# Kernel optimization log

Hardware: AMD Instinct MI355X
Metric: run time of the kernel (lower is better)

Reference implementation:

```python
import jax, jax.numpy as jnp
import numpy as np

CODEBOOK_SIZE = 1024
EMBEDDING_DIM = 64


def setup_inputs() -> dict:
    key = jax.random.key(0)
    k_in, k_cb = jax.random.split(key)
    # latent feature (batch, embedding_dim, length)
    input = jax.random.normal(k_in, (16, EMBEDDING_DIM, 8192), dtype=jnp.float32)
    # learned codebook table (codebook_size, embedding_dim)
    codebook = jax.random.normal(k_cb, (CODEBOOK_SIZE, EMBEDDING_DIM), dtype=jnp.float32)
    return {"input": input, "codebook": codebook}


def reference(input, codebook):
    # input: (B, D, T); codebook: (K, D)
    B, D = input.shape[0], input.shape[1]
    spatial = input.shape[2:]
    # move embedding dim last and flatten tokens: (B*T, D)
    x = jnp.moveaxis(input, 1, -1).reshape(-1, D)
    x_sq = jnp.sum(x * x, axis=-1, keepdims=True)            # (N, 1)
    e_sq = jnp.sum(codebook * codebook, axis=-1)             # (K,)
    dist = x_sq - 2.0 * (x @ codebook.T) + e_sq[None, :]     # (N, K)
    indices = jnp.argmin(dist, axis=-1)                      # (N,)
    quantized = jnp.take(codebook, indices, axis=0)          # (N, D)
    # reshape back: output (B, D, *spatial), indices (B, *spatial)
    out = jnp.moveaxis(quantized.reshape((B,) + spatial + (D,)), -1, 1)
    idx = indices.reshape((B,) + spatial)
    return out, idx
```

## Files before the change

### kernel.cpp

```cpp
#include <hip/hip_runtime.h>
#include <float.h>

#define K_CODES 1024
#define DIM 64
#define T_LEN 8192
#define N_TOK 131072
#define LO_SCALE 2048.0f
#define LO_INV   (1.0f / 2048.0f)

typedef _Float16 half8 __attribute__((ext_vector_type(8)));
typedef float    f32x4 __attribute__((ext_vector_type(4)));

#define MFMA16(a, b, c) __builtin_amdgcn_mfma_f32_16x16x32_f16((a), (b), (c), 0, 0, 0)

__global__ void vq_prep(const float* __restrict__ cb,
                        _Float16* __restrict__ w,
                        float* __restrict__ wesq) {
    __shared__ float part[128];
    const int ct   = blockIdx.x;
    const int r    = threadIdx.x;
    const int halF = r >> 7;
    const int rr   = r & 127;
    const int q    = rr >> 4;
    const int code = rr & 15;

    const float* src = cb + (size_t)(ct * 16 + code) * DIM + q * 8;
    float4 v0 = *reinterpret_cast<const float4*>(src);
    float4 v1 = *reinterpret_cast<const float4*>(src + 4);
    float x[8] = {v0.x, v0.y, v0.z, v0.w, v1.x, v1.y, v1.z, v1.w};

    half8 o;
    float psum = 0.0f;
    #pragma unroll
    for (int j = 0; j < 8; ++j) {
        _Float16 h = (_Float16)x[j];
        o[j] = halF ? (_Float16)((x[j] - (float)h) * LO_SCALE) : h;
        psum = fmaf(x[j], x[j], psum);
    }
    *reinterpret_cast<half8*>(w + (size_t)ct * 2048 + halF * 1024 + q * 128 + code * 8) = o;

    if (halF == 0) part[rr] = psum;
    __syncthreads();
    if (r < 16) {
        float s = 0.0f;
        #pragma unroll
        for (int q2 = 0; q2 < 8; ++q2) s += part[q2 * 16 + r];
        wesq[ct * 16 + r] = s;
    }
}

__global__ __launch_bounds__(256, 4)
void vq_main(const float* __restrict__ in,
             const float* __restrict__ cb,
             const _Float16* __restrict__ w,
             const float* __restrict__ wesq,
             float* __restrict__ out) {
    __shared__ int idx_s[128];

    const int tid  = threadIdx.x;
    const int wave = tid >> 6;
    const int lane = tid & 63;
    const int lo4  = lane & 15;
    const int quad = lane >> 4;

    const int strip = blockIdx.x * 128 + wave * 32;
    const int b  = strip >> 13;
    const int t0 = strip & 8191;

    const float* xin = in + (size_t)b * DIM * T_LEN + t0;
    half8 a_hi[2][2], a_lo[2][2];
    #pragma unroll
    for (int mt = 0; mt < 2; ++mt) {
        #pragma unroll
        for (int s = 0; s < 2; ++s) {
            half8 hh, ll;
            #pragma unroll
            for (int j = 0; j < 8; ++j) {
                const int d = s * 32 + quad * 8 + j;
                float xv = -2.0f * xin[(size_t)d * T_LEN + mt * 16 + lo4];
                _Float16 h = (_Float16)xv;
                hh[j] = h;
                ll[j] = (_Float16)((xv - (float)h) * LO_SCALE);
            }
            a_hi[mt][s] = hh;
            a_lo[mt][s] = ll;
        }
    }

    float best[8];
    int   bidx[8];
    #pragma unroll
    for (int i = 0; i < 8; ++i) { best[i] = FLT_MAX; bidx[i] = 0; }

    const _Float16* wb = w + (size_t)lane * 8;

    half8 Ah0, Ah1, Al0, Al1, Bh0, Bh1, Bl0, Bl1;
    float Ae, Be;

    auto loadB = [&](int ct, half8& h0, half8& h1, half8& l0, half8& l1, float& es) {
        const _Float16* p = wb + (size_t)ct * 2048;
        h0 = *reinterpret_cast<const half8*>(p);
        h1 = *reinterpret_cast<const half8*>(p + 512);
        l0 = *reinterpret_cast<const half8*>(p + 1024);
        l1 = *reinterpret_cast<const half8*>(p + 1536);
        es = wesq[ct * 16 + lo4];
    };
    auto step = [&](const half8& h0, const half8& h1, const half8& l0,
                    const half8& l1, float es, int ct) {
        const int code = ct * 16 + lo4;
        #pragma unroll
        for (int mt = 0; mt < 2; ++mt) {
            f32x4 c1 = {es, es, es, es};
            f32x4 c2 = {0.f, 0.f, 0.f, 0.f};
            c1 = MFMA16(a_hi[mt][0], h0, c1);
            c1 = MFMA16(a_hi[mt][1], h1, c1);
            c2 = MFMA16(a_lo[mt][0], h0, c2);
            c2 = MFMA16(a_lo[mt][1], h1, c2);
            c2 = MFMA16(a_hi[mt][0], l0, c2);
            c2 = MFMA16(a_hi[mt][1], l1, c2);
            #pragma unroll
            for (int r = 0; r < 4; ++r) {
                float sc = fmaf(c2[r], LO_INV, c1[r]);
                const int i = mt * 4 + r;
                bool lt = sc < best[i];
                best[i] = lt ? sc : best[i];
                bidx[i] = lt ? code : bidx[i];
            }
        }
    };

    loadB(0, Ah0, Ah1, Al0, Al1, Ae);
    loadB(1, Bh0, Bh1, Bl0, Bl1, Be);
    for (int p = 0; p < 31; ++p) {
        step(Ah0, Ah1, Al0, Al1, Ae, 2 * p);
        loadB(2 * p + 2, Ah0, Ah1, Al0, Al1, Ae);
        step(Bh0, Bh1, Bl0, Bl1, Be, 2 * p + 1);
        loadB(2 * p + 3, Bh0, Bh1, Bl0, Bl1, Be);
    }
    step(Ah0, Ah1, Al0, Al1, Ae, 62);
    step(Bh0, Bh1, Bl0, Bl1, Be, 63);

    #pragma unroll
    for (int i = 0; i < 8; ++i) {
        float s = best[i];
        int  ix = bidx[i];
        #pragma unroll
        for (int off = 1; off < 16; off <<= 1) {
            float s2 = __shfl_xor(s, off, 64);
            int  ix2 = __shfl_xor(ix, off, 64);
            bool take = (s2 < s) || (s2 == s && ix2 < ix);
            s  = take ? s2 : s;
            ix = take ? ix2 : ix;
        }
        if (lo4 == 0) {
            idx_s[wave * 32 + (i >> 2) * 16 + quad * 4 + (i & 3)] = ix;
        }
    }
    __syncthreads();

    const int tok_local = tid & 127;
    const int dhalf = tid >> 7;
    const int token = blockIdx.x * 128 + tok_local;
    const int tb = token >> 13;
    const int tt = token & 8191;
    const int my_idx = idx_s[tok_local];

    if (dhalf == 0)
        out[(size_t)N_TOK * DIM + token] = (float)my_idx;

    const float* crow = cb + (size_t)my_idx * DIM + dhalf * 32;
    float* outv = out + (size_t)tb * DIM * T_LEN + (size_t)(dhalf * 32) * T_LEN + tt;
    #pragma unroll
    for (int d0 = 0; d0 < 32; d0 += 4) {
        float4 v = *reinterpret_cast<const float4*>(crow + d0);
        outv[(size_t)(d0 + 0) * T_LEN] = v.x;
        outv[(size_t)(d0 + 1) * T_LEN] = v.y;
        outv[(size_t)(d0 + 2) * T_LEN] = v.z;
        outv[(size_t)(d0 + 3) * T_LEN] = v.w;
    }
}

extern "C" void kernel_launch(void* const* d_in, const int* in_sizes, int n_in,
                              void* d_out, int out_size, void* d_ws, size_t ws_size,
                              hipStream_t stream) {
    const float* in = (const float*)d_in[0];
    const float* cb = (const float*)d_in[1];
    float* out = (float*)d_out;

    _Float16* w   = (_Float16*)d_ws;
    float*   wesq = (float*)((char*)d_ws + 64 * 4096);

    vq_prep<<<dim3(64), dim3(256), 0, stream>>>(cb, w, wesq);
    vq_main<<<dim3(N_TOK / 128), dim3(256), 0, stream>>>(in, cb, w, wesq, out);
}
```

Before: 134.0 us.

## Stage codebook tiles in LDS via async global-to-LDS double buffering

Instead of every wave loading the same split-fp16 codebook tiles from global memory into registers, the block cooperatively copies 4 tiles at a time into a double-buffered LDS area using global_load_lds. Each wave then reads its fragments from LDS, with one barrier per period. The codebook squared norms are also preloaded into LDS. This cuts redundant L2/global traffic by sharing loads across the 4 waves. The cost is extra LDS use (about 36 KB per block, which may limit occupancy), LDS read latency and per-period barriers.

Result: slower. 139.5 us (+4.1%).

```diff
diff --git a/kernel.cpp b/kernel.cpp
--- a/kernel.cpp
+++ b/kernel.cpp
@@ -12,6 +12,17 @@
 typedef float    f32x4 __attribute__((ext_vector_type(4)));
 
 #define MFMA16(a, b, c) __builtin_amdgcn_mfma_f32_16x16x32_f16((a), (b), (c), 0, 0, 0)
+
+typedef __attribute__((address_space(3))) void* as3_void;
+typedef const __attribute__((address_space(1))) void* as1_cvoid;
+
+__device__ inline void async_16B(const void* g, void* l) {
+#if __has_builtin(__builtin_amdgcn_global_load_lds)
+    __builtin_amdgcn_global_load_lds((as1_cvoid)g, (as3_void)l, 16, 0, 0);
+#else
+    *(float4*)l = *(const float4*)g;
+#endif
+}
 
 __global__ void vq_prep(const float* __restrict__ cb,
                         _Float16* __restrict__ w,
@@ -55,13 +66,17 @@
              const _Float16* __restrict__ w,
              const float* __restrict__ wesq,
              float* __restrict__ out) {
-    __shared__ int idx_s[128];
+    __shared__ __align__(16) _Float16 bt[2][4][2048];
+    __shared__ float esq_s[K_CODES];
+    __shared__ int   idx_s[128];
 
     const int tid  = threadIdx.x;
     const int wave = tid >> 6;
     const int lane = tid & 63;
     const int lo4  = lane & 15;
     const int quad = lane >> 4;
+
+    for (int k = tid; k < K_CODES; k += 256) esq_s[k] = wesq[k];
 
     const int strip = blockIdx.x * 128 + wave * 32;
     const int b  = strip >> 13;
@@ -92,53 +107,55 @@
     #pragma unroll
     for (int i = 0; i < 8; ++i) { best[i] = FLT_MAX; bidx[i] = 0; }
 
-    const _Float16* wb = w + (size_t)lane * 8;
-
-    half8 Ah0, Ah1, Al0, Al1, Bh0, Bh1, Bl0, Bl1;
-    float Ae, Be;
-
-    auto loadB = [&](int ct, half8& h0, half8& h1, half8& l0, half8& l1, float& es) {
-        const _Float16* p = wb + (size_t)ct * 2048;
-        h0 = *reinterpret_cast<const half8*>(p);
-        h1 = *reinterpret_cast<const half8*>(p + 512);
-        l0 = *reinterpret_cast<const half8*>(p + 1024);
-        l1 = *reinterpret_cast<const half8*>(p + 1536);
-        es = wesq[ct * 16 + lo4];
+    const char* wbytes = (const char*)w;
+    auto stage = [&](int per, int buf) {
+        const char* src = wbytes + (size_t)per * 16384 + lane * 16;
+        char* dst = (char*)&bt[buf][0][0] + lane * 16;
+        #pragma unroll
+        for (int i = 0; i < 4; ++i) {
+            const int c = (wave + i * 4) * 1024;
+            async_16B(src + c, dst + c);
+        }
     };
-    auto step = [&](const half8& h0, const half8& h1, const half8& l0,
-                    const half8& l1, float es, int ct) {
-        const int code = ct * 16 + lo4;
-        #pragma unroll
-        for (int mt = 0; mt < 2; ++mt) {
-            f32x4 c1 = {es, es, es, es};
-            f32x4 c2 = {0.f, 0.f, 0.f, 0.f};
-            c1 = MFMA16(a_hi[mt][0], h0, c1);
-            c1 = MFMA16(a_hi[mt][1], h1, c1);
-            c2 = MFMA16(a_lo[mt][0], h0, c2);
-            c2 = MFMA16(a_lo[mt][1], h1, c2);
-            c2 = MFMA16(a_hi[mt][0], l0, c2);
-            c2 = MFMA16(a_hi[mt][1], l1, c2);
+
+    stage(0, 0);
+    __syncthreads();
+
+    for (int per = 0; per < 16; ++per) {
+        const int buf = per & 1;
+        if (per < 15) stage(per + 1, buf ^ 1);
+        #pragma unroll
+        for (int j = 0; j < 4; ++j) {
+            const int ct = per * 4 + j;
+            const _Float16* tp = &bt[buf][j][lane * 8];
+            half8 h0 = *reinterpret_cast<const half8*>(tp);
+            half8 h1 = *reinterpret_cast<const half8*>(tp + 512);
+            half8 l0 = *reinterpret_cast<const half8*>(tp + 1024);
+            half8 l1 = *reinterpret_cast<const half8*>(tp + 1536);
+            const float es = esq_s[ct * 16 + lo4];
+            const int code = ct * 16 + lo4;
             #pragma unroll
-            for (int r = 0; r < 4; ++r) {
-                float sc = fmaf(c2[r], LO_INV, c1[r]);
-                const int i = mt * 4 + r;
-                bool lt = sc < best[i];
-                best[i] = lt ? sc : best[i];
-                bidx[i] = lt ? code : bidx[i];
+            for (int mt = 0; mt < 2; ++mt) {
+                f32x4 c1 = {es, es, es, es};
+                f32x4 c2 = {0.f, 0.f, 0.f, 0.f};
+                c1 = MFMA16(a_hi[mt][0], h0, c1);
+                c1 = MFMA16(a_hi[mt][1], h1, c1);
+                c2 = MFMA16(a_lo[mt][0], h0, c2);
+                c2 = MFMA16(a_lo[mt][1], h1, c2);
+                c2 = MFMA16(a_hi[mt][0], l0, c2);
+                c2 = MFMA16(a_hi[mt][1], l1, c2);
+                #pragma unroll
+                for (int r = 0; r < 4; ++r) {
+                    float sc = fmaf(c2[r], LO_INV, c1[r]);
+                    const int i = mt * 4 + r;
+                    bool lt = sc < best[i];
+                    best[i] = lt ? sc : best[i];
+                    bidx[i] = lt ? code : bidx[i];
+                }
             }
         }
-    };
-
-    loadB(0, Ah0, Ah1, Al0, Al1, Ae);
-    loadB(1, Bh0, Bh1, Bl0, Bl1, Be);
-    for (int p = 0; p < 31; ++p) {
-        step(Ah0, Ah1, Al0, Al1, Ae, 2 * p);
-        loadB(2 * p + 2, Ah0, Ah1, Al0, Al1, Ae);
-        step(Bh0, Bh1, Bl0, Bl1, Be, 2 * p + 1);
-        loadB(2 * p + 3, Bh0, Bh1, Bl0, Bl1, Be);
-    }
-    step(Ah0, Ah1, Al0, Al1, Ae, 62);
-    step(Bh0, Bh1, Bl0, Bl1, Be, 63);
+        __syncthreads();
+    }
 
     #pragma unroll
     for (int i = 0; i < 8; ++i) {
```

## Double tokens per wave, fold hi/lo split into one scaled accumulator, stage esq in LDS

Applied to the files above, without the earlier changes.

Each wave now handles 64 tokens (4 M-tiles) instead of 32, so every codebook B-fragment loaded from global memory is reused across twice as many MFMAs. The two accumulator chains (hi and lo, combined with an fmaf) become a single chain: the high part of the input is pre-scaled by 2048 and the codebook norms are stored pre-scaled, so the argmin works on scaled distances without the per-element combine. Codebook norms are staged in shared memory, and the grid is halved with launch bounds relaxed to allow more registers. The costs are higher register pressure and lower occupancy. Scaling the high fp16 part by 2048 could also overflow fp16 for large inputs.

New measurement: 128.2 us. 1.05x faster.

```diff
diff --git a/kernel.cpp b/kernel.cpp
--- a/kernel.cpp
+++ b/kernel.cpp
@@ -6,7 +6,6 @@
 #define T_LEN 8192
 #define N_TOK 131072
 #define LO_SCALE 2048.0f
-#define LO_INV   (1.0f / 2048.0f)
 
 typedef _Float16 half8 __attribute__((ext_vector_type(8)));
 typedef float    f32x4 __attribute__((ext_vector_type(4)));
@@ -45,17 +44,18 @@
         float s = 0.0f;
         #pragma unroll
         for (int q2 = 0; q2 < 8; ++q2) s += part[q2 * 16 + r];
-        wesq[ct * 16 + r] = s;
+        wesq[ct * 16 + r] = s * LO_SCALE;
     }
 }
 
-__global__ __launch_bounds__(256, 4)
+__global__ __launch_bounds__(256, 2)
 void vq_main(const float* __restrict__ in,
              const float* __restrict__ cb,
              const _Float16* __restrict__ w,
              const float* __restrict__ wesq,
              float* __restrict__ out) {
-    __shared__ int idx_s[128];
+    __shared__ float esq_s[K_CODES];
+    __shared__ int   idx_s[256];
 
     const int tid  = threadIdx.x;
     const int wave = tid >> 6;
@@ -63,64 +63,67 @@
     const int lo4  = lane & 15;
     const int quad = lane >> 4;
 
-    const int strip = blockIdx.x * 128 + wave * 32;
+    for (int k = tid; k < K_CODES; k += 256) esq_s[k] = wesq[k];
+    __syncthreads();
+
+    const int strip = blockIdx.x * 256 + wave * 64;
     const int b  = strip >> 13;
     const int t0 = strip & 8191;
 
     const float* xin = in + (size_t)b * DIM * T_LEN + t0;
-    half8 a_hi[2][2], a_lo[2][2];
+    half8 a_h[4][2], a_hs[4][2], a_l[4][2];
     #pragma unroll
-    for (int mt = 0; mt < 2; ++mt) {
+    for (int mt = 0; mt < 4; ++mt) {
         #pragma unroll
         for (int s = 0; s < 2; ++s) {
-            half8 hh, ll;
+            half8 hh, hs, ll;
             #pragma unroll
             for (int j = 0; j < 8; ++j) {
                 const int d = s * 32 + quad * 8 + j;
                 float xv = -2.0f * xin[(size_t)d * T_LEN + mt * 16 + lo4];
                 _Float16 h = (_Float16)xv;
                 hh[j] = h;
+                hs[j] = (_Float16)((float)h * LO_SCALE);
                 ll[j] = (_Float16)((xv - (float)h) * LO_SCALE);
             }
-            a_hi[mt][s] = hh;
-            a_lo[mt][s] = ll;
+            a_h[mt][s] = hh;
+            a_hs[mt][s] = hs;
+            a_l[mt][s] = ll;
         }
     }
 
-    float best[8];
-    int   bidx[8];
+    float best[16];
+    int   bidx[16];
     #pragma unroll
-    for (int i = 0; i < 8; ++i) { best[i] = FLT_MAX; bidx[i] = 0; }
+    for (int i = 0; i < 16; ++i) { best[i] = FLT_MAX; bidx[i] = 0; }
 
     const _Float16* wb = w + (size_t)lane * 8;
 
     half8 Ah0, Ah1, Al0, Al1, Bh0, Bh1, Bl0, Bl1;
     float Ae, Be;
-
     auto loadB = [&](int ct, half8& h0, half8& h1, half8& l0, half8& l1, float& es) {
         const _Float16* p = wb + (size_t)ct * 2048;
         h0 = *reinterpret_cast<const half8*>(p);
         h1 = *reinterpret_cast<const half8*>(p + 512);
         l0 = *reinterpret_cast<const half8*>(p + 1024);
         l1 = *reinterpret_cast<const half8*>(p + 1536);
-        es = wesq[ct * 16 + lo4];
+        es = esq_s[ct * 16 + lo4];
     };
     auto step = [&](const half8& h0, const half8& h1, const half8& l0,
                     const half8& l1, float es, int ct) {
         const int code = ct * 16 + lo4;
         #pragma unroll
-        for (int mt = 0; mt < 2; ++mt) {
-            f32x4 c1 = {es, es, es, es};
-            f32x4 c2 = {0.f, 0.f, 0.f, 0.f};
-            c1 = MFMA16(a_hi[mt][0], h0, c1);
-            c1 = MFMA16(a_hi[mt][1], h1, c1);
-            c2 = MFMA16(a_lo[mt][0], h0, c2);
-            c2 = MFMA16(a_lo[mt][1], h1, c2);
-            c2 = MFMA16(a_hi[mt][0], l0, c2);
-            c2 = MFMA16(a_hi[mt][1], l1, c2);
+        for (int mt = 0; mt < 4; ++mt) {
+            f32x4 c = {es, es, es, es};
+            c = MFMA16(a_hs[mt][0], h0, c);
+            c = MFMA16(a_hs[mt][1], h1, c);
+            c = MFMA16(a_h[mt][0], l0, c);
+            c = MFMA16(a_h[mt][1], l1, c);
+            c = MFMA16(a_l[mt][0], h0, c);
+            c = MFMA16(a_l[mt][1], h1, c);
             #pragma unroll
             for (int r = 0; r < 4; ++r) {
-                float sc = fmaf(c2[r], LO_INV, c1[r]);
+                float sc = c[r];
                 const int i = mt * 4 + r;
                 bool lt = sc < best[i];
                 best[i] = lt ? sc : best[i];
@@ -141,7 +144,7 @@
     step(Bh0, Bh1, Bl0, Bl1, Be, 63);
 
     #pragma unroll
-    for (int i = 0; i < 8; ++i) {
+    for (int i = 0; i < 16; ++i) {
         float s = best[i];
         int  ix = bidx[i];
         #pragma unroll
@@ -153,25 +156,22 @@
             ix = take ? ix2 : ix;
         }
         if (lo4 == 0) {
-            idx_s[wave * 32 + (i >> 2) * 16 + quad * 4 + (i & 3)] = ix;
+            idx_s[wave * 64 + (i >> 2) * 16 + quad * 4 + (i & 3)] = ix;
         }
     }
     __syncthreads();
 
-    const int tok_local = tid & 127;
-    const int dhalf = tid >> 7;
-    const int token = blockIdx.x * 128 + tok_local;
+    const int token = blockIdx.x * 256 + tid;
     const int tb = token >> 13;
     const int tt = token & 8191;
-    const int my_idx = idx_s[tok_local];
+    const int my_idx = idx_s[tid];
 
-    if (dhalf == 0)
-        out[(size_t)N_TOK * DIM + token] = (float)my_idx;
+    out[(size_t)N_TOK * DIM + token] = (float)my_idx;
 
-    const float* crow = cb + (size_t)my_idx * DIM + dhalf * 32;
-    float* outv = out + (size_t)tb * DIM * T_LEN + (size_t)(dhalf * 32) * T_LEN + tt;
+    const float* crow = cb + (size_t)my_idx * DIM;
+    float* outv = out + (size_t)tb * DIM * T_LEN + tt;
     #pragma unroll
-    for (int d0 = 0; d0 < 32; d0 += 4) {
+    for (int d0 = 0; d0 < DIM; d0 += 4) {
         float4 v = *reinterpret_cast<const float4*>(crow + d0);
         outv[(size_t)(d0 + 0) * T_LEN] = v.x;
         outv[(size_t)(d0 + 1) * T_LEN] = v.y;
@@ -191,5 +191,5 @@
     float*   wesq = (float*)((char*)d_ws + 64 * 4096);
 
     vq_prep<<<dim3(64), dim3(256), 0, stream>>>(cb, w, wesq);
-    vq_main<<<dim3(N_TOK / 128), dim3(256), 0, stream>>>(in, cb, w, wesq, out);
+    vq_main<<<dim3(N_TOK / 256), dim3(256), 0, stream>>>(in, cb, w, wesq, out);
 }
```
